# Kernel optimization log

Hardware: AMD Instinct MI355X
Metric: run time of the kernel (lower is better)

## Reference

```python
import jax, jax.numpy as jnp
import numpy as np

DIM = 4096
N_HEADS = 32
N_KV_HEADS = 8
HEAD_DIM = DIM // N_HEADS  # 128
N_REP = N_HEADS // N_KV_HEADS  # 4
SEQ = 2048
BLOCK = 64
N_BLK = SEQ // BLOCK  # 32
TOPK = 8
NEG = -1e30


def _rope(x, cos, sin):
    # x: (B, L, H, D); cos/sin: (L, D/2). Pairs are interleaved (..., D/2, 2)
    B, L, H, D = x.shape
    xr = x.reshape(B, L, H, D // 2, 2)
    x0, x1 = xr[..., 0], xr[..., 1]
    c = cos[None, :, None, :]
    s = sin[None, :, None, :]
    o0 = x0 * c - x1 * s
    o1 = x0 * s + x1 * c
    return jnp.stack([o0, o1], axis=-1).reshape(B, L, H, D)


def setup_inputs() -> dict:
    key = jax.random.key(0)
    ks = jax.random.split(key, 8)
    x = jax.random.normal(ks[0], (1, SEQ, DIM), dtype=jnp.float32)
    # true RoPE angles (theta = 10000^{-2i/D})
    inv_freq = 1.0 / (10000.0 ** (np.arange(0, HEAD_DIM, 2, dtype=np.float32) / HEAD_DIM))
    angles = np.arange(SEQ, dtype=np.float32)[:, None] * inv_freq[None, :]  # (L, D/2)
    cos = jnp.asarray(np.cos(angles))
    sin = jnp.asarray(np.sin(angles))
    sc = 0.02
    wq = jax.random.normal(ks[1], (DIM, N_HEADS * HEAD_DIM), dtype=jnp.float32) * sc
    wk = jax.random.normal(ks[2], (DIM, N_KV_HEADS * HEAD_DIM), dtype=jnp.float32) * sc
    wv = jax.random.normal(ks[3], (DIM, N_KV_HEADS * HEAD_DIM), dtype=jnp.float32) * sc
    wo = jax.random.normal(ks[4], (N_HEADS * HEAD_DIM, DIM), dtype=jnp.float32) * sc
    return {"x": x, "cos": cos, "sin": sin, "wq": wq, "wk": wk, "wv": wv, "wo": wo}


def reference(x, cos, sin, wq, wk, wv, wo):
    B, L, _ = x.shape
    # QKV projections
    q = (x @ wq).reshape(B, L, N_HEADS, HEAD_DIM)
    k = (x @ wk).reshape(B, L, N_KV_HEADS, HEAD_DIM)
    v = (x @ wv).reshape(B, L, N_KV_HEADS, HEAD_DIM)
    # rotary embeddings on q and k
    q = _rope(q, cos, sin)
    k = _rope(k, cos, sin)
    # GQA: expand kv heads n_rep times
    k = jnp.repeat(k, N_REP, axis=2)  # (B, L, Hq, D)
    v = jnp.repeat(v, N_REP, axis=2)
    q = q.transpose(0, 2, 1, 3)  # (B, H, L, D)
    k = k.transpose(0, 2, 1, 3)
    v = v.transpose(0, 2, 1, 3)
    scale = 1.0 / jnp.sqrt(jnp.asarray(HEAD_DIM, dtype=q.dtype))

    pos = jnp.arange(L)
    causal = pos[None, :] <= pos[:, None]  # (Lq, Lk): key <= query

    # Block representatives: mean key per block -> top-k block selection per query
    k_blk = k.reshape(B, N_HEADS, N_BLK, BLOCK, HEAD_DIM).mean(axis=3)  # (B,H,Nblk,D)
    blk_scores = jnp.einsum('bhqd,bhnd->bhqn', q, k_blk) * scale  # (B,H,L,Nblk)
    blk_start = jnp.arange(N_BLK) * BLOCK
    blk_allowed = blk_start[None, :] <= pos[:, None]  # (L, Nblk)
    blk_scores = jnp.where(blk_allowed[None, None], blk_scores, NEG)
    _, top_idx = jax.lax.top_k(blk_scores, TOPK)  # (B,H,L,TOPK)
    blk_mask = jax.nn.one_hot(top_idx, N_BLK, dtype=jnp.bool_).any(axis=-2)  # (B,H,L,Nblk)

    # Expand block mask to per-key mask, combine with causal
    key_mask = jnp.repeat(blk_mask, BLOCK, axis=-1)  # (B,H,L,S)
    key_mask = key_mask & causal[None, None]

    scores = jnp.einsum('bhqd,bhkd->bhqk', q, k) * scale  # (B,H,L,S)
    scores = jnp.where(key_mask, scores, NEG)
    attn = jax.nn.softmax(scores, axis=-1)
    out = jnp.einsum('bhqk,bhkd->bhqd', attn, v)  # (B,H,L,D)
    out = out.transpose(0, 2, 1, 3).reshape(B, L, N_HEADS * HEAD_DIM)
    return out @ wo
```

## Files before the change

kernel.cpp:

```cpp
#include <hip/hip_runtime.h>
#include <hip/hip_bf16.h>
#include <math.h>

#define SEQ 2048
#define DIM 4096
#define NH 32
#define HD 128
#define NKV 8
#define NREP 4
#define BLOCK 64
#define NBLK 32
#define TOPK 8
#define KVDIM (NKV * HD)
#define SCALE 0.08838834764831845f

__device__ inline unsigned short f2b(float f) {
    __hip_bfloat16 h = __float2bfloat16(f);
    return *reinterpret_cast<unsigned short*>(&h);
}
__device__ inline float bitsf(unsigned int u) {
    union { float f; unsigned int i; } x; x.i = u; return x.f;
}
__device__ inline float b2f(unsigned short us) { return bitsf(((unsigned int)us) << 16); }
__device__ inline void unpack2(unsigned int w0, float* o) {
    o[0] = bitsf(w0 << 16);
    o[1] = bitsf(w0 & 0xffff0000u);
}
__device__ inline void unpack4(uint2 w, float* o) { unpack2(w.x, o); unpack2(w.y, o + 2); }
__device__ inline void unpack8(uint4 w, float* o) {
    unpack2(w.x, o); unpack2(w.y, o + 2); unpack2(w.z, o + 4); unpack2(w.w, o + 6);
}
__device__ inline float dot4f(float4 a, float4 b) {
    return a.x * b.x + a.y * b.y + a.z * b.z + a.w * b.w;
}

typedef __attribute__((ext_vector_type(8))) short bfrag;
typedef __attribute__((ext_vector_type(4))) float ffrag;

__device__ __forceinline__ void gl_lds16(const void* g, void* l) {
    __builtin_amdgcn_global_load_lds((const __attribute__((address_space(1))) void*)g,
                                     (__attribute__((address_space(3))) void*)l, 16, 0, 0);
}

template <bool SPLIT>
__global__ __launch_bounds__(256) void mfma_gemm(const unsigned short* __restrict__ Ah,
                                                 const unsigned short* __restrict__ Al,
                                                 const unsigned short* __restrict__ Bh,
                                                 const unsigned short* __restrict__ Bl,
                                                 float* __restrict__ C,
                                                 int M, int N, int K) {
    __shared__ short As[(SPLIT ? 2 : 1) * 4096];
    __shared__ short Bs[(SPLIT ? 2 : 1) * 4096];

    const int tid = threadIdx.x;
    const int lane = tid & 63;
    const int w = tid >> 6;
    const int wm = (w >> 1) * 64;
    const int wn = (w & 1) * 64;
    const int m = lane & 15;
    const int quad = lane >> 4;

    int bx = blockIdx.x, by = blockIdx.y;
    {
        const int nwg = gridDim.x * gridDim.y;
        if ((nwg & 7) == 0) {
            const int flat = by * gridDim.x + bx;
            const int nper = nwg >> 3;
            const int swz = (flat & 7) * nper + (flat >> 3);
            bx = swz % gridDim.x;
            by = swz / gridDim.x;
        }
    }
    const int bm = by * 128;
    const int bn = bx * 128;

    const int r0 = tid >> 2;
    const int c0 = (tid & 3) * 8;
    const size_t aoff0 = (size_t)(bm + r0) * K + c0;
    const size_t aoff1 = (size_t)(bm + r0 + 64) * K + c0;
    const size_t boff0 = (size_t)(bn + r0) * K + c0;
    const size_t boff1 = (size_t)(bn + r0 + 64) * K + c0;

    ffrag acc[4][4];
    const ffrag z = {0.f, 0.f, 0.f, 0.f};
#pragma unroll
    for (int i = 0; i < 4; ++i)
#pragma unroll
        for (int j = 0; j < 4; ++j) acc[i][j] = z;

    for (int kt = 0; kt < K; kt += 32) {
        __syncthreads();
        gl_lds16(Ah + aoff0 + kt, As + tid * 8);
        gl_lds16(Ah + aoff1 + kt, As + 2048 + tid * 8);
        gl_lds16(Bh + boff0 + kt, Bs + tid * 8);
        gl_lds16(Bh + boff1 + kt, Bs + 2048 + tid * 8);
        if constexpr (SPLIT) {
            gl_lds16(Al + aoff0 + kt, As + 4096 + tid * 8);
            gl_lds16(Al + aoff1 + kt, As + 6144 + tid * 8);
            gl_lds16(Bl + boff0 + kt, Bs + 4096 + tid * 8);
            gl_lds16(Bl + boff1 + kt, Bs + 6144 + tid * 8);
        }
        __syncthreads();

        bfrag ah[4], bh[4];
#pragma unroll
        for (int i = 0; i < 4; ++i)
            ah[i] = *(const bfrag*)(As + (wm + i * 16 + m) * 32 + quad * 8);
#pragma unroll
        for (int j = 0; j < 4; ++j)
            bh[j] = *(const bfrag*)(Bs + (wn + j * 16 + m) * 32 + quad * 8);
        if constexpr (SPLIT) {
            bfrag al[4], bl[4];
#pragma unroll
            for (int i = 0; i < 4; ++i)
                al[i] = *(const bfrag*)(As + 4096 + (wm + i * 16 + m) * 32 + quad * 8);
#pragma unroll
            for (int j = 0; j < 4; ++j)
                bl[j] = *(const bfrag*)(Bs + 4096 + (wn + j * 16 + m) * 32 + quad * 8);
#pragma unroll
            for (int i = 0; i < 4; ++i)
#pragma unroll
                for (int j = 0; j < 4; ++j) {
                    acc[i][j] = __builtin_amdgcn_mfma_f32_16x16x32_bf16(ah[i], bh[j], acc[i][j], 0, 0, 0);
                    acc[i][j] = __builtin_amdgcn_mfma_f32_16x16x32_bf16(ah[i], bl[j], acc[i][j], 0, 0, 0);
                    acc[i][j] = __builtin_amdgcn_mfma_f32_16x16x32_bf16(al[i], bh[j], acc[i][j], 0, 0, 0);
                }
        } else {
#pragma unroll
            for (int i = 0; i < 4; ++i)
#pragma unroll
                for (int j = 0; j < 4; ++j)
                    acc[i][j] = __builtin_amdgcn_mfma_f32_16x16x32_bf16(ah[i], bh[j], acc[i][j], 0, 0, 0);
        }
    }

#pragma unroll
    for (int i = 0; i < 4; ++i)
#pragma unroll
        for (int j = 0; j < 4; ++j)
#pragma unroll
            for (int r = 0; r < 4; ++r)
                C[(size_t)(bm + wm + i * 16 + quad * 4 + r) * N + bn + wn + j * 16 + m] =
                    acc[i][j][r];
}

__global__ __launch_bounds__(256) void transpose_conv(const float* __restrict__ W,
                                                      unsigned short* __restrict__ Th,
                                                      unsigned short* __restrict__ Tl,
                                                      int K, int N, int rowoff) {
    __shared__ float tile[32][36];
    const int k0 = blockIdx.y * 32, n0 = blockIdx.x * 32;
    const int t = threadIdx.x;
    const int r = t >> 3, c4 = (t & 7) * 4;
    *(float4*)&tile[r][c4] = *(const float4*)(W + (size_t)(k0 + r) * N + n0 + c4);
    __syncthreads();
    float v0 = tile[c4 + 0][r], v1 = tile[c4 + 1][r], v2 = tile[c4 + 2][r], v3 = tile[c4 + 3][r];
    ushort4 h;
    h.x = f2b(v0); h.y = f2b(v1); h.z = f2b(v2); h.w = f2b(v3);
    const size_t ooff = (size_t)(rowoff + n0 + r) * K + k0 + c4;
    *(ushort4*)(Th + ooff) = h;
    if (Tl) {
        ushort4 l;
        l.x = f2b(v0 - b2f(h.x)); l.y = f2b(v1 - b2f(h.y));
        l.z = f2b(v2 - b2f(h.z)); l.w = f2b(v3 - b2f(h.w));
        *(ushort4*)(Tl + ooff) = l;
    }
}

__global__ void conv_hilo(const float* __restrict__ X, unsigned short* __restrict__ H,
                          unsigned short* __restrict__ L) {
    const int i = (blockIdx.x * blockDim.x + threadIdx.x) * 4;
    const float4 x = *(const float4*)(X + i);
    ushort4 h;
    h.x = f2b(x.x); h.y = f2b(x.y); h.z = f2b(x.z); h.w = f2b(x.w);
    *(ushort4*)(H + i) = h;
    if (L) {
        ushort4 l;
        l.x = f2b(x.x - b2f(h.x)); l.y = f2b(x.y - b2f(h.y));
        l.z = f2b(x.z - b2f(h.z)); l.w = f2b(x.w - b2f(h.w));
        *(ushort4*)(L + i) = l;
    }
}

__global__ void kconv_kernel(const float* __restrict__ kvf, unsigned short* __restrict__ kb) {
    const int i = (blockIdx.x * blockDim.x + threadIdx.x) * 4;
    const int s = i >> 10, c = i & 1023;
    const float4 x = *(const float4*)(kvf + (size_t)s * 2048 + c);
    ushort4 h;
    h.x = f2b(x.x); h.y = f2b(x.y); h.z = f2b(x.z); h.w = f2b(x.w);
    *(ushort4*)(kb + (size_t)s * 1024 + c) = h;
}

__global__ __launch_bounds__(256) void vtrans_kernel(const float* __restrict__ kvf,
                                                     unsigned short* __restrict__ vt) {
    __shared__ unsigned short tile[64][72];
    const int s0 = blockIdx.x * 64;
    const int c0 = blockIdx.y * 64;
    const int t = threadIdx.x;
    const int r = t >> 4;
    const int c4 = (t & 15) * 4;
#pragma unroll
    for (int u = 0; u < 4; ++u) {
        const float4 x = *(const float4*)(kvf + (size_t)(s0 + u * 16 + r) * 2048 + 1024 + c0 + c4);
        ushort4 hh;
        hh.x = f2b(x.x); hh.y = f2b(x.y); hh.z = f2b(x.z); hh.w = f2b(x.w);
        *(ushort4*)(&tile[u * 16 + r][c4]) = hh;
    }
    __syncthreads();
    const int cc = t >> 2;
    const int sg = (t & 3) * 16;
    union { unsigned short s[16]; uint4 v[2]; } bb;
#pragma unroll
    for (int i = 0; i < 16; ++i) bb.s[i] = tile[sg + i][cc];
    unsigned short* op = vt + (size_t)(c0 + cc) * 2048 + s0 + sg;
    *(uint4*)op = bb.v[0];
    *(uint4*)(op + 8) = bb.v[1];
}

__global__ __launch_bounds__(256) void gemm_kernel(const float* __restrict__ A,
                                                   const float* __restrict__ B,
                                                   float* __restrict__ C,
                                                   int M, int N, int K) {
    __shared__ __align__(16) float As[16][68];
    __shared__ __align__(16) float Bs[16][68];

    const int tid = threadIdx.x;
    const int bm = blockIdx.y * 64;
    const int bn = blockIdx.x * 64;
    const int tm = (tid >> 4) * 4;
    const int tn = (tid & 15) * 4;

    float acc[4][4] = {};

    for (int k0 = 0; k0 < K; k0 += 16) {
        {
            const int mm = tid >> 2;
            const int kk = (tid & 3) * 4;
            const float* ap = A + (size_t)(bm + mm) * K + k0 + kk;
            const float4 a4 = *reinterpret_cast<const float4*>(ap);
            As[kk + 0][mm] = a4.x;
            As[kk + 1][mm] = a4.y;
            As[kk + 2][mm] = a4.z;
            As[kk + 3][mm] = a4.w;
        }
        {
            const int kk = tid >> 4;
            const int n = (tid & 15) * 4;
            const float* bp = B + (size_t)(k0 + kk) * N + bn + n;
            *reinterpret_cast<float4*>(&Bs[kk][n]) = *reinterpret_cast<const float4*>(bp);
        }
        __syncthreads();
#pragma unroll
        for (int kk = 0; kk < 16; ++kk) {
            const float4 a4 = *reinterpret_cast<const float4*>(&As[kk][tm]);
            const float4 b4 = *reinterpret_cast<const float4*>(&Bs[kk][tn]);
            const float av[4] = {a4.x, a4.y, a4.z, a4.w};
            const float bv[4] = {b4.x, b4.y, b4.z, b4.w};
#pragma unroll
            for (int i = 0; i < 4; ++i)
#pragma unroll
                for (int j = 0; j < 4; ++j) acc[i][j] += av[i] * bv[j];
        }
        __syncthreads();
    }
#pragma unroll
    for (int i = 0; i < 4; ++i)
#pragma unroll
        for (int j = 0; j < 4; ++j)
            C[(size_t)(bm + tm + i) * N + bn + tn + j] = acc[i][j];
}

__global__ void rope_kernel(float* __restrict__ x, const float* __restrict__ cosb,
                            const float* __restrict__ sinb, int nh, int stride) {
    const int idx = blockIdx.x * blockDim.x + threadIdx.x;
    const int i = idx & 63;
    const int h = (idx >> 6) % nh;
    const int pos = idx / (64 * nh);
    const float c = cosb[pos * 64 + i];
    const float s = sinb[pos * 64 + i];
    float* p = x + (size_t)pos * stride + h * HD + 2 * i;
    const float x0 = p[0], x1 = p[1];
    p[0] = x0 * c - x1 * s;
    p[1] = x0 * s + x1 * c;
}

__global__ void blkmean_kernel(const float* __restrict__ k, float* __restrict__ kblk,
                               int stride) {
    const int idx = blockIdx.x * blockDim.x + threadIdx.x;
    const int d = idx & 127;
    const int blk = (idx >> 7) & 31;
    const int kv = idx >> 12;
    float s = 0.f;
#pragma unroll 8
    for (int r = 0; r < BLOCK; ++r)
        s += k[(size_t)(blk * BLOCK + r) * stride + kv * HD + d];
    kblk[idx] = s * (1.f / 64.f);
}

__global__ __launch_bounds__(256, 3) void attn_mfma_kernel(const float* __restrict__ q,
                                                           const unsigned short* __restrict__ kbp,
                                                           const unsigned short* __restrict__ vtp,
                                                           const float* __restrict__ kblk,
                                                           float* __restrict__ out) {
    __shared__ __align__(16) unsigned char smem[45568];
    unsigned short* ksb = (unsigned short*)smem;
    unsigned short* vsb = (unsigned short*)(smem + 17408);
    unsigned short* psb = (unsigned short*)(smem + 35840);
    unsigned int*  selm = (unsigned int*)(smem + 45056);
    float* kbf = (float*)smem;
    float* bsc = (float*)(smem + 16896);

    int bx = blockIdx.x, by = blockIdx.y;
    {
        const int flat = by * 32 + bx;
        const int swz = (flat & 7) * 128 + (flat >> 3);
        bx = swz & 31;
        by = swz >> 5;
    }
    const int qt = 31 - bx;
    const int h = by;
    const int kv = h >> 2;
    const int qbase = qt * 64;
    const int tid = threadIdx.x;
    const int lane = tid & 63;
    const int w = tid >> 6;
    const int m = lane & 15;
    const int quad = lane >> 4;
    const int wm = w * 16;

    unsigned int uni;
    if (qt + 1 > TOPK) {
#pragma unroll
        for (int u = 0; u < 4; ++u) {
            const int idx = u * 1024 + tid * 4;
            const int b = idx >> 7, d = idx & 127;
            *(float4*)(kbf + b * 132 + d) =
                *(const float4*)(kblk + ((size_t)(kv * NBLK + b)) * HD + d);
        }
        __syncthreads();
        {
            float acc[4][2] = {};
            const int r0 = quad + 4 * w;
#pragma unroll 4
            for (int d = 0; d < 128; d += 4) {
                float4 qv[4], kb2[2];
#pragma unroll
                for (int i = 0; i < 4; ++i)
                    qv[i] = *(const float4*)(q + ((size_t)((qbase + r0 + 16 * i) * NH + h)) * HD + d);
#pragma unroll
                for (int j = 0; j < 2; ++j) kb2[j] = *(float4*)(kbf + (m + 16 * j) * 132 + d);
#pragma unroll
                for (int i = 0; i < 4; ++i)
#pragma unroll
                    for (int j = 0; j < 2; ++j) acc[i][j] += dot4f(qv[i], kb2[j]);
            }
#pragma unroll
            for (int i = 0; i < 4; ++i)
#pragma unroll
                for (int j = 0; j < 2; ++j) {
                    const int b = m + 16 * j;
                    if (b <= qt) bsc[(r0 + 16 * i) * 33 + b] = acc[i][j];
                }
        }
        __syncthreads();
        if (tid < 64) {
            unsigned int sel = 0;
            const float* br = bsc + tid * 33;
            for (int t2 = 0; t2 < TOPK; ++t2) {
                float best = -3.4e38f; int bi = 0;
                for (int b = 0; b <= qt; ++b)
                    if (!((sel >> b) & 1u) && br[b] > best) { best = br[b]; bi = b; }
                sel |= 1u << bi;
            }
            selm[tid] = sel;
        }
        __syncthreads();
        unsigned int u2 = 0;
        for (int i = 0; i < 64; ++i) u2 |= selm[i];
        uni = u2;
    } else {
        uni = (2u << qt) - 1;
    }

    unsigned int selr[4];
#pragma unroll
    for (int r = 0; r < 4; ++r)
        selr[r] = (qt + 1 > TOPK) ? selm[wm + quad * 4 + r] : uni;

    bfrag aq[4];
    {
        const float* qrow = q + ((size_t)((qbase + wm + m) * NH + h)) * HD;
#pragma unroll
        for (int ks = 0; ks < 4; ++ks) {
            const float4 f0 = *(const float4*)(qrow + ks * 32 + quad * 8);
            const float4 f1 = *(const float4*)(qrow + ks * 32 + quad * 8 + 4);
            bfrag a;
            a[0] = (short)f2b(f0.x); a[1] = (short)f2b(f0.y);
            a[2] = (short)f2b(f0.z); a[3] = (short)f2b(f0.w);
            a[4] = (short)f2b(f1.x); a[5] = (short)f2b(f1.y);
            a[6] = (short)f2b(f1.z); a[7] = (short)f2b(f1.w);
            aq[ks] = a;
        }
    }

    float m_run[4], l_run[4];
#pragma unroll
    for (int r = 0; r < 4; ++r) { m_run[r] = -3.0e38f; l_run[r] = 0.f; }
    ffrag o[8];
    const ffrag z = {0.f, 0.f, 0.f, 0.f};
#pragma unroll
    for (int n = 0; n < 8; ++n) o[n] = z;

    unsigned short* psw = psb + w * (16 * 72);

    uint4 kreg[4], vreg[4];
    unsigned int rem = uni;
    if (rem) {
        const int b0 = __builtin_ctz(rem);
#pragma unroll
        for (int u = 0; u < 4; ++u) {
            const int idx = u * 256 + tid;
            kreg[u] = *(const uint4*)(kbp + (size_t)(b0 * 64 + (idx >> 4)) * 1024 + kv * 128 + (idx & 15) * 8);
        }
#pragma unroll
        for (int u = 0; u < 4; ++u) {
            const int idx = u * 256 + tid;
            vreg[u] = *(const uint4*)(vtp + (size_t)(kv * 128 + (idx >> 3)) * 2048 + b0 * 64 + (idx & 7) * 8);
        }
    }

    while (rem) {
        const int b = __builtin_ctz(rem);
        rem &= rem - 1;
        __syncthreads();
#pragma unroll
        for (int u = 0; u < 4; ++u) {
            const int idx = u * 256 + tid;
            *(uint4*)(ksb + (idx >> 4) * 136 + (idx & 15) * 8) = kreg[u];
        }
#pragma unroll
        for (int u = 0; u < 4; ++u) {
            const int idx = u * 256 + tid;
            *(uint4*)(vsb + (idx >> 3) * 72 + (idx & 7) * 8) = vreg[u];
        }
        const bool hn = (rem != 0);
        const int bn = hn ? __builtin_ctz(rem) : 0;
        __syncthreads();
        if (hn) {
#pragma unroll
            for (int u = 0; u < 4; ++u) {
                const int idx = u * 256 + tid;
                kreg[u] = *(const uint4*)(kbp + (size_t)(bn * 64 + (idx >> 4)) * 1024 + kv * 128 + (idx & 15) * 8);
            }
#pragma unroll
            for (int u = 0; u < 4; ++u) {
                const int idx = u * 256 + tid;
                vreg[u] = *(const uint4*)(vtp + (size_t)(kv * 128 + (idx >> 3)) * 2048 + bn * 64 + (idx & 7) * 8);
            }
        }

        ffrag s[4];
#pragma unroll
        for (int j = 0; j < 4; ++j) s[j] = z;
        __builtin_amdgcn_s_setprio(1);
#pragma unroll
        for (int ks = 0; ks < 4; ++ks) {
#pragma unroll
            for (int j = 0; j < 4; ++j) {
                const bfrag bk = *(const bfrag*)(ksb + (j * 16 + m) * 136 + ks * 32 + quad * 8);
                s[j] = __builtin_amdgcn_mfma_f32_16x16x32_bf16(aq[ks], bk, s[j], 0, 0, 0);
            }
        }
        __builtin_amdgcn_s_setprio(0);

        const bool diag = (b == qt);
        float a_r[4];
#pragma unroll
        for (int r = 0; r < 4; ++r) {
            const int rloc = quad * 4 + r;
            const int rtile = wm + rloc;
            const bool selb = (selr[r] >> b) & 1u;
            float sv[4];
#pragma unroll
            for (int j = 0; j < 4; ++j) {
                const int col = j * 16 + m;
                const bool valid = selb && (!diag || col <= rtile);
                sv[j] = valid ? s[j][r] * SCALE : -3.0e38f;
            }
            float t = fmaxf(fmaxf(sv[0], sv[1]), fmaxf(sv[2], sv[3]));
            t = fmaxf(t, __shfl_xor(t, 1));
            t = fmaxf(t, __shfl_xor(t, 2));
            t = fmaxf(t, __shfl_xor(t, 4));
            t = fmaxf(t, __shfl_xor(t, 8));
            const float mo = m_run[r];
            const float mn = fmaxf(mo, t);
            a_r[r] = __expf(mo - mn);
            float sum = 0.f;
#pragma unroll
            for (int j = 0; j < 4; ++j) {
                const float p = (sv[j] > -1.0e30f) ? __expf(sv[j] - mn) : 0.f;
                psw[rloc * 72 + j * 16 + m] = f2b(p);
                sum += p;
            }
            sum += __shfl_xor(sum, 1);
            sum += __shfl_xor(sum, 2);
            sum += __shfl_xor(sum, 4);
            sum += __shfl_xor(sum, 8);
            l_run[r] = l_run[r] * a_r[r] + sum;
            m_run[r] = mn;
        }
#pragma unroll
        for (int n = 0; n < 8; ++n)
#pragma unroll
            for (int r = 0; r < 4; ++r) o[n][r] *= a_r[r];

        __builtin_amdgcn_s_setprio(1);
#pragma unroll
        for (int ks = 0; ks < 2; ++ks) {
            const bfrag pa = *(const bfrag*)(psw + m * 72 + ks * 32 + quad * 8);
#pragma unroll
            for (int n = 0; n < 8; ++n) {
                const bfrag bv = *(const bfrag*)(vsb + (n * 16 + m) * 72 + ks * 32 + quad * 8);
                o[n] = __builtin_amdgcn_mfma_f32_16x16x32_bf16(pa, bv, o[n], 0, 0, 0);
            }
        }
        __builtin_amdgcn_s_setprio(0);
    }

#pragma unroll
    for (int r = 0; r < 4; ++r) {
        const float inv = 1.f / l_run[r];
        float* op = out + ((size_t)((qbase + wm + quad * 4 + r) * NH + h)) * HD + m;
#pragma unroll
        for (int n = 0; n < 8; ++n) op[n * 16] = o[n][r] * inv;
    }
}

__global__ __launch_bounds__(256) void attn_tile_kernel(const float* __restrict__ q,
                                                        const float* __restrict__ kptr,
                                                        const float* __restrict__ vptr,
                                                        const float* __restrict__ kblk,
                                                        float* __restrict__ out,
                                                        int kvstride) {
    __shared__ __align__(16) unsigned char smem[62464];
    unsigned short* ksb = (unsigned short*)smem;
    unsigned short* vsb = (unsigned short*)(smem + 17408);
    unsigned short* psb = (unsigned short*)(smem + 34816);
    unsigned short* qsb = (unsigned short*)(smem + 43520);
    float* mrow = (float*)(smem + 60928);
    float* lrow = (float*)(smem + 61184);
    float* arow = (float*)(smem + 61440);
    float* mnew = (float*)(smem + 61696);
    unsigned int* selm = (unsigned int*)(smem + 61952);
    float* qf  = (float*)smem;
    float* kbf = (float*)(smem + 33792);
    float* bsc = (float*)(smem + 50688);

    const int qt = 31 - blockIdx.x;
    const int h = blockIdx.y;
    const int kv = h >> 2;
    const int qbase = qt * 64;
    const int tid = threadIdx.x;
    const int lane = tid & 63;
    const int w = tid >> 6;
    const int kl = lane & 15;
    const int ql = lane >> 4;

#pragma unroll
    for (int u = 0; u < 8; ++u) {
        const int idx = u * 1024 + tid * 4;
        const int qi = idx >> 7, d = idx & 127;
        *(float4*)(qf + qi * 132 + d) =
            *(const float4*)(q + ((size_t)((qbase + qi) * NH + h)) * HD + d);
    }
#pragma unroll
    for (int u = 0; u < 4; ++u) {
        const int idx = u * 1024 + tid * 4;
        const int b = idx >> 7, d = idx & 127;
        *(float4*)(kbf + b * 132 + d) =
            *(const float4*)(kblk + ((size_t)(kv * NBLK + b)) * HD + d);
    }
    __syncthreads();

    {
        float acc[4][2] = {};
#pragma unroll 4
        for (int d = 0; d < 128; d += 4) {
            float4 qv[4], kb2[2];
#pragma unroll
            for (int i = 0; i < 4; ++i) qv[i] = *(float4*)(qf + (ql + 4 * w + 16 * i) * 132 + d);
#pragma unroll
            for (int j = 0; j < 2; ++j) kb2[j] = *(float4*)(kbf + (kl + 16 * j) * 132 + d);
#pragma unroll
            for (int i = 0; i < 4; ++i)
#pragma unroll
                for (int j = 0; j < 2; ++j) acc[i][j] += dot4f(qv[i], kb2[j]);
        }
#pragma unroll
        for (int i = 0; i < 4; ++i)
#pragma unroll
            for (int j = 0; j < 2; ++j) {
                const int b = kl + 16 * j;
                if (b <= qt) bsc[(ql + 4 * w + 16 * i) * 33 + b] = acc[i][j];
            }
    }
    __syncthreads();

    if (tid < 64) {
        const int ns = (qt + 1 < TOPK) ? qt + 1 : TOPK;
        unsigned int sel = 0;
        const float* br = bsc + tid * 33;
        for (int t = 0; t < ns; ++t) {
            float best = -3.4e38f; int bi = 0;
            for (int b = 0; b <= qt; ++b)
                if (!((sel >> b) & 1u) && br[b] > best) { best = br[b]; bi = b; }
            sel |= 1u << bi;
        }
        selm[tid] = sel;
        mrow[tid] = -3.0e38f;
        lrow[tid] = 0.f;
    }
    __syncthreads();

    unsigned int uni = 0;
    {
        float tmp[32];
#pragma unroll
        for (int u = 0; u < 8; ++u) {
            const int idx = u * 1024 + tid * 4;
            *(float4*)(tmp + u * 4) = *(float4*)(qf + (idx >> 7) * 132 + (idx & 127));
        }
        for (int i = 0; i < 64; ++i) uni |= selm[i];
#pragma unroll
        for (int u = 0; u < 8; ++u) {
            const int idx = u * 1024 + tid * 4;
            const int qi = idx >> 7, d = idx & 127;
            ushort4 qu;
            qu.x = f2b(tmp[u * 4 + 0]); qu.y = f2b(tmp[u * 4 + 1]);
            qu.z = f2b(tmp[u * 4 + 2]); qu.w = f2b(tmp[u * 4 + 3]);
            *(ushort4*)(qsb + qi * 136 + d) = qu;
        }
    }
    __syncthreads();

    const int qi_r[4] = {ql + 4 * w, ql + 4 * w + 16, ql + 4 * w + 32, ql + 4 * w + 48};
    unsigned int selq[4];
#pragma unroll
    for (int i = 0; i < 4; ++i) selq[i] = selm[qi_r[i]];

    float O[4][8] = {};

    for (int b = 0; b <= qt; ++b) {
        if (!((uni >> b) & 1u)) continue;
        __syncthreads();
#pragma unroll
        for (int u = 0; u < 8; ++u) {
            const int idx = u * 1024 + tid * 4;
            const int r = idx >> 7, d = idx & 127;
            const size_t gof = (size_t)(b * 64 + r) * kvstride + kv * HD + d;
            const float4 k4 = *(const float4*)(kptr + gof);
            const float4 v4 = *(const float4*)(vptr + gof);
            ushort4 ku, vu;
            ku.x = f2b(k4.x); ku.y = f2b(k4.y); ku.z = f2b(k4.z); ku.w = f2b(k4.w);
            vu.x = f2b(v4.x); vu.y = f2b(v4.y); vu.z = f2b(v4.z); vu.w = f2b(v4.w);
            *(ushort4*)(ksb + r * 136 + d) = ku;
            *(ushort4*)(vsb + r * 136 + d) = vu;
        }
        __syncthreads();

        float S[4][4] = {};
#pragma unroll 4
        for (int d = 0; d < 128; d += 4) {
            float qv[4][4], kk4[4][4];
#pragma unroll
            for (int i = 0; i < 4; ++i) unpack4(*(uint2*)(qsb + qi_r[i] * 136 + d), qv[i]);
#pragma unroll
            for (int j = 0; j < 4; ++j) unpack4(*(uint2*)(ksb + (kl + 16 * j) * 136 + d), kk4[j]);
#pragma unroll
            for (int i = 0; i < 4; ++i)
#pragma unroll
                for (int j = 0; j < 4; ++j)
#pragma unroll
                    for (int e = 0; e < 4; ++e) S[i][j] += qv[i][e] * kk4[j][e];
        }

        const bool diag = (b == qt);
        float tm[4];
#pragma unroll
        for (int i = 0; i < 4; ++i) {
            const bool selb = (selq[i] >> b) & 1u;
#pragma unroll
            for (int j = 0; j < 4; ++j) {
                const int kj = kl + 16 * j;
                const bool valid = selb && (!diag || kj <= qi_r[i]);
                S[i][j] = valid ? S[i][j] * SCALE : -3.0e38f;
            }
            float t = fmaxf(fmaxf(S[i][0], S[i][1]), fmaxf(S[i][2], S[i][3]));
            t = fmaxf(t, __shfl_xor(t, 1));
            t = fmaxf(t, __shfl_xor(t, 2));
            t = fmaxf(t, __shfl_xor(t, 4));
            t = fmaxf(t, __shfl_xor(t, 8));
            tm[i] = t;
        }
        if (kl == 0) {
#pragma unroll
            for (int i = 0; i < 4; ++i) {
                const float mo = mrow[qi_r[i]];
                const float mn = fmaxf(mo, tm[i]);
                mrow[qi_r[i]] = mn;
                mnew[qi_r[i]] = mn;
                arow[qi_r[i]] = __expf(mo - mn);
            }
        }
        __syncthreads();

        float tl[4];
#pragma unroll
        for (int i = 0; i < 4; ++i) {
            const float mn = mnew[qi_r[i]];
            float sum = 0.f;
#pragma unroll
            for (int j = 0; j < 4; ++j) {
                const float p = (S[i][j] > -1.0e30f) ? __expf(S[i][j] - mn) : 0.f;
                psb[qi_r[i] * 68 + kl + 16 * j] = f2b(p);
                sum += p;
            }
            sum += __shfl_xor(sum, 1);
            sum += __shfl_xor(sum, 2);
            sum += __shfl_xor(sum, 4);
            sum += __shfl_xor(sum, 8);
            tl[i] = sum;
        }
        if (kl == 0) {
#pragma unroll
            for (int i = 0; i < 4; ++i)
                lrow[qi_r[i]] = lrow[qi_r[i]] * arow[qi_r[i]] + tl[i];
        }
#pragma unroll
        for (int i = 0; i < 4; ++i) {
            const float a = arow[qi_r[i]];
#pragma unroll
            for (int e = 0; e < 8; ++e) O[i][e] *= a;
        }
        __syncthreads();

#pragma unroll 4
        for (int kj = 0; kj < 64; ++kj) {
            float p[4];
#pragma unroll
            for (int i = 0; i < 4; ++i) {
                unsigned short us = psb[qi_r[i] * 68 + kj];
                p[i] = bitsf(((unsigned int)us) << 16);
            }
            float vv[8];
            unpack8(*(uint4*)(vsb + kj * 136 + kl * 8), vv);
#pragma unroll
            for (int i = 0; i < 4; ++i)
#pragma unroll
                for (int e = 0; e < 8; ++e) O[i][e] += p[i] * vv[e];
        }
    }
    __syncthreads();

#pragma unroll
    for (int i = 0; i < 4; ++i) {
        const float inv = 1.f / lrow[qi_r[i]];
        float4 o0, o1;
        o0.x = O[i][0] * inv; o0.y = O[i][1] * inv; o0.z = O[i][2] * inv; o0.w = O[i][3] * inv;
        o1.x = O[i][4] * inv; o1.y = O[i][5] * inv; o1.z = O[i][6] * inv; o1.w = O[i][7] * inv;
        float* op = out + ((size_t)((qbase + qi_r[i]) * NH + h)) * HD + kl * 8;
        *(float4*)op = o0;
        *(float4*)(op + 4) = o1;
    }
}

extern "C" void kernel_launch(void* const* d_in, const int* in_sizes, int n_in,
                              void* d_out, int out_size, void* d_ws, size_t ws_size,
                              hipStream_t stream) {
    const float* x    = (const float*)d_in[0];
    const float* cosb = (const float*)d_in[1];
    const float* sinb = (const float*)d_in[2];
    const float* wq   = (const float*)d_in[3];
    const float* wk   = (const float*)d_in[4];
    const float* wv   = (const float*)d_in[5];
    const float* wo   = (const float*)d_in[6];

    unsigned char* ws = (unsigned char*)d_ws;
    const dim3 t256(256);

    const size_t MAIN_REQ = 184680448ull;
    if (ws_size >= MAIN_REQ) {
        float*          qf     = (float*)(ws);
        float*          kvf    = (float*)(ws + 33554432ull);
        float*          kblk   = (float*)(ws + 50331648ull);
        unsigned short* x_hi   = (unsigned short*)(ws + 50462720ull);
        unsigned short* x_lo   = (unsigned short*)(ws + 67239936ull);
        float*          attn   = (float*)(ws + 50462720ull);
        unsigned short* wqT_hi = (unsigned short*)(ws + 84017152ull);
        unsigned short* wqT_lo = (unsigned short*)(ws + 117571584ull);
        unsigned short* kvT_hi = (unsigned short*)(ws + 151126016ull);
        unsigned short* kvT_lo = (unsigned short*)(ws + 167903232ull);
        unsigned short* woT_hi = wqT_hi;
        unsigned short* attnbf = wqT_lo;
        unsigned short* kb16   = kvT_hi;
        unsigned short* vtb    = kvT_lo;

        conv_hilo<<<SEQ * DIM / 4 / 256, t256, 0, stream>>>(x, x_hi, x_lo);
        transpose_conv<<<dim3(DIM / 32, DIM / 32), t256, 0, stream>>>(wq, wqT_hi, wqT_lo, DIM, DIM, 0);
        transpose_conv<<<dim3(KVDIM / 32, DIM / 32), t256, 0, stream>>>(wk, kvT_hi, kvT_lo, DIM, KVDIM, 0);
        transpose_conv<<<dim3(KVDIM / 32, DIM / 32), t256, 0, stream>>>(wv, kvT_hi, kvT_lo, DIM, KVDIM, KVDIM);

        hipLaunchKernelGGL((mfma_gemm<true>), dim3(DIM / 128, SEQ / 128), t256, 0, stream,
                           x_hi, x_lo, wqT_hi, wqT_lo, qf, SEQ, DIM, DIM);
        hipLaunchKernelGGL((mfma_gemm<true>), dim3(2 * KVDIM / 128, SEQ / 128), t256, 0, stream,
                           x_hi, x_lo, kvT_hi, kvT_lo, kvf, SEQ, 2 * KVDIM, DIM);
        transpose_conv<<<dim3(DIM / 32, DIM / 32), t256, 0, stream>>>(wo, woT_hi, nullptr, DIM, DIM, 0);

        rope_kernel<<<(SEQ * NH * 64) / 256, t256, 0, stream>>>(qf, cosb, sinb, NH, NH * HD);
        rope_kernel<<<(SEQ * NKV * 64) / 256, t256, 0, stream>>>(kvf, cosb, sinb, NKV, 2 * KVDIM);
        blkmean_kernel<<<(NKV * NBLK * HD) / 256, t256, 0, stream>>>(kvf, kblk, 2 * KVDIM);

        kconv_kernel<<<(SEQ * KVDIM / 4) / 256, t256, 0, stream>>>(kvf, kb16);
        vtrans_kernel<<<dim3(SEQ / 64, KVDIM / 64), t256, 0, stream>>>(kvf, vtb);

        attn_mfma_kernel<<<dim3(NBLK, NH), t256, 0, stream>>>(qf, kb16, vtb, kblk, attn);

        conv_hilo<<<SEQ * DIM / 4 / 256, t256, 0, stream>>>(attn, attnbf, nullptr);
        hipLaunchKernelGGL((mfma_gemm<false>), dim3(DIM / 128, SEQ / 128), t256, 0, stream,
                           attnbf, nullptr, woT_hi, nullptr, (float*)d_out, SEQ, DIM, DIM);
    } else {
        float* qf   = (float*)ws;
        float* kf   = qf + (size_t)SEQ * DIM;
        float* vf   = kf + (size_t)SEQ * KVDIM;
        float* kblk = vf + (size_t)SEQ * KVDIM;
        float* attn = kblk + (size_t)NKV * NBLK * HD;

        gemm_kernel<<<dim3(DIM / 64, SEQ / 64), t256, 0, stream>>>(x, wq, qf, SEQ, DIM, DIM);
        gemm_kernel<<<dim3(KVDIM / 64, SEQ / 64), t256, 0, stream>>>(x, wk, kf, SEQ, KVDIM, DIM);
        gemm_kernel<<<dim3(KVDIM / 64, SEQ / 64), t256, 0, stream>>>(x, wv, vf, SEQ, KVDIM, DIM);
        rope_kernel<<<(SEQ * NH * 64) / 256, t256, 0, stream>>>(qf, cosb, sinb, NH, NH * HD);
        rope_kernel<<<(SEQ * NKV * 64) / 256, t256, 0, stream>>>(kf, cosb, sinb, NKV, KVDIM);
        blkmean_kernel<<<(NKV * NBLK * HD) / 256, t256, 0, stream>>>(kf, kblk, KVDIM);
        attn_tile_kernel<<<dim3(NBLK, NH), t256, 0, stream>>>(qf, kf, vf, kblk, attn, KVDIM);
        gemm_kernel<<<dim3(DIM / 64, SEQ / 64), t256, 0, stream>>>(attn, wo, (float*)d_out, SEQ, DIM, DIM);
    }
}
```

Measured before the change: 979.8 us.

## Load K/V tiles directly to LDS with XOR swizzle, drop register prefetch

Replaces the register-staged double-buffered prefetch of K and V tiles with direct global-to-LDS loads into an XOR-swizzled unpadded layout, and adjusts the fragment reads to match. This removes staging registers and padding, which may raise occupancy and avoid bank conflicts. The next block is no longer prefetched during compute, so load latency is exposed each iteration unless other waves hide it.

```diff
diff --git a/kernel.cpp b/kernel.cpp
--- a/kernel.cpp
+++ b/kernel.cpp
@@ -297,16 +297,16 @@
     kblk[idx] = s * (1.f / 64.f);
 }
 
-__global__ __launch_bounds__(256, 3) void attn_mfma_kernel(const float* __restrict__ q,
-                                                           const unsigned short* __restrict__ kbp,
-                                                           const unsigned short* __restrict__ vtp,
-                                                           const float* __restrict__ kblk,
-                                                           float* __restrict__ out) {
-    __shared__ __align__(16) unsigned char smem[45568];
+__global__ __launch_bounds__(256) void attn_mfma_kernel(const float* __restrict__ q,
+                                                        const unsigned short* __restrict__ kbp,
+                                                        const unsigned short* __restrict__ vtp,
+                                                        const float* __restrict__ kblk,
+                                                        float* __restrict__ out) {
+    __shared__ __align__(16) unsigned char smem[42240];
     unsigned short* ksb = (unsigned short*)smem;
-    unsigned short* vsb = (unsigned short*)(smem + 17408);
-    unsigned short* psb = (unsigned short*)(smem + 35840);
-    unsigned int*  selm = (unsigned int*)(smem + 45056);
+    unsigned short* vsb = (unsigned short*)(smem + 16384);
+    unsigned short* psb = (unsigned short*)(smem + 32768);
+    unsigned int*  selm = (unsigned int*)(smem + 41984);
     float* kbf = (float*)smem;
     float* bsc = (float*)(smem + 16896);
 
@@ -412,52 +412,31 @@
     for (int n = 0; n < 8; ++n) o[n] = z;
 
     unsigned short* psw = psb + w * (16 * 72);
-
-    uint4 kreg[4], vreg[4];
+    const int xorm = (m & 7) << 4;
+
     unsigned int rem = uni;
-    if (rem) {
-        const int b0 = __builtin_ctz(rem);
-#pragma unroll
-        for (int u = 0; u < 4; ++u) {
-            const int idx = u * 256 + tid;
-            kreg[u] = *(const uint4*)(kbp + (size_t)(b0 * 64 + (idx >> 4)) * 1024 + kv * 128 + (idx & 15) * 8);
-        }
-#pragma unroll
-        for (int u = 0; u < 4; ++u) {
-            const int idx = u * 256 + tid;
-            vreg[u] = *(const uint4*)(vtp + (size_t)(kv * 128 + (idx >> 3)) * 2048 + b0 * 64 + (idx & 7) * 8);
-        }
-    }
-
     while (rem) {
         const int b = __builtin_ctz(rem);
         rem &= rem - 1;
         __syncthreads();
+
 #pragma unroll
         for (int u = 0; u < 4; ++u) {
-            const int idx = u * 256 + tid;
-            *(uint4*)(ksb + (idx >> 4) * 136 + (idx & 15) * 8) = kreg[u];
+            const int L = (u * 256 + tid) * 16;
+            const int row = L >> 8;
+            const int sc = (L ^ ((row & 7) << 4)) & 255;
+            gl_lds16(kbp + (size_t)(b * 64 + row) * 1024 + kv * 128 + (sc >> 1),
+                     (unsigned char*)smem + L);
         }
 #pragma unroll
         for (int u = 0; u < 4; ++u) {
-            const int idx = u * 256 + tid;
-            *(uint4*)(vsb + (idx >> 3) * 72 + (idx & 7) * 8) = vreg[u];
-        }
-        const bool hn = (rem != 0);
-        const int bn = hn ? __builtin_ctz(rem) : 0;
-        __syncthreads();
-        if (hn) {
-#pragma unroll
-            for (int u = 0; u < 4; ++u) {
-                const int idx = u * 256 + tid;
-                kreg[u] = *(const uint4*)(kbp + (size_t)(bn * 64 + (idx >> 4)) * 1024 + kv * 128 + (idx & 15) * 8);
-            }
-#pragma unroll
-            for (int u = 0; u < 4; ++u) {
-                const int idx = u * 256 + tid;
-                vreg[u] = *(const uint4*)(vtp + (size_t)(kv * 128 + (idx >> 3)) * 2048 + bn * 64 + (idx & 7) * 8);
-            }
-        }
+            const int L = (u * 256 + tid) * 16;
+            const int row = L >> 7;
+            const int sc = (L ^ ((row & 7) << 4)) & 127;
+            gl_lds16(vtp + (size_t)(kv * 128 + row) * 2048 + b * 64 + (sc >> 1),
+                     (unsigned char*)smem + 16384 + L);
+        }
+        __syncthreads();
 
         ffrag s[4];
 #pragma unroll
@@ -467,7 +446,8 @@
         for (int ks = 0; ks < 4; ++ks) {
 #pragma unroll
             for (int j = 0; j < 4; ++j) {
-                const bfrag bk = *(const bfrag*)(ksb + (j * 16 + m) * 136 + ks * 32 + quad * 8);
+                const int kb = (((j * 16 + m) << 8) + (ks << 6) + (quad << 4)) ^ xorm;
+                const bfrag bk = *(const bfrag*)((const unsigned char*)ksb + kb);
                 s[j] = __builtin_amdgcn_mfma_f32_16x16x32_bf16(aq[ks], bk, s[j], 0, 0, 0);
             }
         }
@@ -520,7 +500,8 @@
             const bfrag pa = *(const bfrag*)(psw + m * 72 + ks * 32 + quad * 8);
 #pragma unroll
             for (int n = 0; n < 8; ++n) {
-                const bfrag bv = *(const bfrag*)(vsb + (n * 16 + m) * 72 + ks * 32 + quad * 8);
+                const int vb = (((n * 16 + m) << 7) + (ks << 6) + (quad << 4)) ^ xorm;
+                const bfrag bv = *(const bfrag*)((const unsigned char*)vsb + vb);
                 o[n] = __builtin_amdgcn_mfma_f32_16x16x32_bf16(pa, bv, o[n], 0, 0, 0);
             }
         }
```

Measured after the change: 887.2 us. 9.5% less time.
